# Performance work log

Hardware: AMD Instinct MI355X
Metric: run time of the kernel (lower is better)

The kernel has to match this reference:

```python
import jax, jax.numpy as jnp
import numpy as np

B = 16384
WIDE_DIM = 256          # 32 wide features * dim 8
DEEP_DIM = 1024         # 64 deep features * embedding_dim 16
SHARED = [2048, 1024, 512]
DOMAIN = [512, 256]
NUM_DOMAINS = 8


def setup_inputs() -> dict:
    key = jax.random.key(0)
    ks = jax.random.split(key, 20)
    s = 0.01  # embedding_init_var-style small init
    inp = {
        "wide_features": jax.random.normal(ks[0], (B, WIDE_DIM), jnp.float32),
        "deep_features": jax.random.normal(ks[1], (B, DEEP_DIM), jnp.float32),
        "domain_ids": jax.random.randint(ks[2], (B,), 0, NUM_DOMAINS, jnp.int64),
        # shared MLP (weights stored [in, out])
        "W1": jax.random.normal(ks[3], (DEEP_DIM, SHARED[0]), jnp.float32) * s,
        "b1": jnp.zeros((SHARED[0],), jnp.float32),
        "W2": jax.random.normal(ks[4], (SHARED[0], SHARED[1]), jnp.float32) * s,
        "b2": jnp.zeros((SHARED[1],), jnp.float32),
        "W3": jax.random.normal(ks[5], (SHARED[1], SHARED[2]), jnp.float32) * s,
        "b3": jnp.zeros((SHARED[2],), jnp.float32),
        # domain-specific MLP
        "Wd1": jax.random.normal(ks[6], (SHARED[2], DOMAIN[0]), jnp.float32) * s,
        "bd1": jnp.zeros((DOMAIN[0],), jnp.float32),
        "Wd2": jax.random.normal(ks[7], (DOMAIN[0], DOMAIN[1]), jnp.float32) * s,
        "bd2": jnp.zeros((DOMAIN[1],), jnp.float32),
        # per-domain output heads: Linear(DOMAIN[-1], 1) per domain
        "Wh": jax.random.normal(ks[8], (NUM_DOMAINS, DOMAIN[1]), jnp.float32) * s,
        "bh": jnp.zeros((NUM_DOMAINS,), jnp.float32),
    }
    return inp


def reference(wide_features, deep_features, domain_ids,
              W1, b1, W2, b2, W3, b3, Wd1, bd1, Wd2, bd2, Wh, bh):
    # wide part: sum embedding output to a scalar logit per sample [B, 1]
    wide = jnp.sum(wide_features, axis=1, keepdims=True)
    # shared deep MLP
    h = jax.nn.relu(deep_features @ W1 + b1)
    h = jax.nn.relu(h @ W2 + b2)
    shared = jax.nn.relu(h @ W3 + b3)          # [B, 512]
    # domain-specific tower (shared across domains)
    d = jax.nn.relu(shared @ Wd1 + bd1)
    d = jax.nn.relu(d @ Wd2 + bd2)             # [B, 256]
    # per-sample domain head routing: gather head weights, fused dot
    w = Wh[domain_ids]                          # [B, 256]
    head = jnp.sum(d * w, axis=1, keepdims=True) + bh[domain_ids][:, None]  # [B, 1]
    out = jax.nn.sigmoid(wide + head)
    return (out, shared, d)
```

## Files before the change

kernel.cpp:

```cpp
#include <hip/hip_runtime.h>
#include <hip/hip_bf16.h>


typedef __attribute__((ext_vector_type(8))) short short8;
typedef __attribute__((ext_vector_type(4))) float f32x4;

static __device__ __forceinline__ unsigned short f2bf_bits(float x) {
  __hip_bfloat16 h = __float2bfloat16(x);
  return __builtin_bit_cast(unsigned short, h);
}
static __device__ __forceinline__ float bf_bits2f(unsigned short u) {
  __hip_bfloat16 h = __builtin_bit_cast(__hip_bfloat16, u);
  return __bfloat162float(h);
}

static __device__ __forceinline__ void gload16(const void* g, void* l) {
  __builtin_amdgcn_global_load_lds(
      (const __attribute__((address_space(1))) void*)g,
      (__attribute__((address_space(3))) void*)l, 16, 0, 0);
}

static __device__ __forceinline__ unsigned lds_u32(const void* p) {
  return (unsigned)(uintptr_t)(const __attribute__((address_space(3))) void*)p;
}

static __device__ __forceinline__ short8 dsr(unsigned addr) {
  short8 r;
  asm volatile("ds_read_b128 %0, %1" : "=v"(r) : "v"(addr));
  return r;
}

#define MFMA16(a, b, c) __builtin_amdgcn_mfma_f32_16x16x32_bf16((a), (b), (c), 0, 0, 0)
#define SB0() __builtin_amdgcn_sched_barrier(0)
#define PRIO(x) __builtin_amdgcn_s_setprio(x)
#define BAR() __builtin_amdgcn_s_barrier()
#define MEMFENCE() asm volatile("" ::: "memory")

__global__ void transpose_convert(const float* __restrict__ W,
                                  __hip_bfloat16* __restrict__ Wt,
                                  int K, int N) {
  __shared__ float tile[64][65];
  const int k0 = blockIdx.y * 64;
  const int n0 = blockIdx.x * 64;
  const int t  = threadIdx.x;
  const int tn = t & 63;
  const int t4 = t >> 6;
#pragma unroll
  for (int p = 0; p < 16; ++p) {
    int kl = p * 4 + t4;
    tile[kl][tn] = W[(size_t)(k0 + kl) * N + (n0 + tn)];
  }
  __syncthreads();
#pragma unroll
  for (int p = 0; p < 16; ++p) {
    int nl = p * 4 + t4;
    Wt[(size_t)(n0 + nl) * K + (k0 + tn)] = __float2bfloat16(tile[tn][nl]);
  }
}

__global__ void f32_to_bf16(const float* __restrict__ in,
                            unsigned short* __restrict__ out, int n8) {
  int i = blockIdx.x * blockDim.x + threadIdx.x;
  if (i >= n8) return;
  const f32x4* p = (const f32x4*)in + (size_t)i * 2;
  f32x4 a = p[0], b = p[1];
  short8 o;
  o[0] = (short)f2bf_bits(a[0]); o[1] = (short)f2bf_bits(a[1]);
  o[2] = (short)f2bf_bits(a[2]); o[3] = (short)f2bf_bits(a[3]);
  o[4] = (short)f2bf_bits(b[0]); o[5] = (short)f2bf_bits(b[1]);
  o[6] = (short)f2bf_bits(b[2]); o[7] = (short)f2bf_bits(b[3]);
  *(short8*)(out + (size_t)i * 8) = o;
}

__global__ __launch_bounds__(512, 2) void gemm_2c(
    const __hip_bfloat16* __restrict__ A,
    const __hip_bfloat16* __restrict__ Bt,
    const float* __restrict__ bias,
    __hip_bfloat16* __restrict__ Cb,
    float* __restrict__ Cf,
    int N, int K, int nbx) {
  __shared__ char lds[131072];

  const int tid  = threadIdx.x;
  const int lane = tid & 63;
  const int wid  = tid >> 6;
  const int wm   = wid >> 2;
  const int wn   = wid & 3;

  const int nwg = gridDim.x;
  const int cpx = nwg >> 3;
  const int id  = blockIdx.x;
  const int swz = (id & 7) * cpx + (id >> 3);
  const int bm  = (swz / nbx) * 256;
  const int bn  = (swz % nbx) * 256;

  const int ln15 = lane & 15;
  const unsigned cswz = (unsigned)((((lane >> 4) ^ (lane & 7)) << 4));

  const unsigned aoff = (unsigned)((wm * 128 + ln15) * 128) + cswz;
  const unsigned boff = 32768u + (unsigned)((wn * 64 + ln15) * 128) + cswz;

  const int nt = K >> 6;

  const __hip_bfloat16* baseA = A  + (size_t)(bm + (tid >> 3)) * K +
                                ((tid & 7) ^ ((tid >> 3) & 7)) * 8;
  const __hip_bfloat16* baseB = Bt + (size_t)(bn + (tid >> 3)) * K +
                                ((tid & 7) ^ ((tid >> 3) & 7)) * 8;
  const unsigned ldst0 = (unsigned)(wid * 1024);

  auto stage = [&](int kt, int half, int isB) {
    const __hip_bfloat16* base = isB ? baseB : baseA;
    char* dst = lds + ((kt & 1) * 65536) + (isB ? 32768 : 0) + half * 16384;
#pragma unroll
    for (int q = 0; q < 2; ++q) {
      gload16(base + (size_t)((half * 128 + q * 64) * K + kt * 64),
              dst + q * 8192 + ldst0);
    }
  };

  auto LD = [&](unsigned off) -> short8 {
    return *(const short8*)&lds[off];
  };

  f32x4 acc[8][4] = {};
  short8 aLo[4][2], aHi[4][2], b0v[2][2], b1v[2][2];

  stage(0, 0, 1); stage(0, 0, 0); stage(0, 1, 1); stage(0, 1, 0);
  if (nt > 1) {
    stage(1, 0, 1); stage(1, 0, 0);
    asm volatile("s_waitcnt vmcnt(4)");
  } else {
    asm volatile("s_waitcnt vmcnt(0)");
  }
  BAR();
  MEMFENCE();
#pragma unroll
  for (int mi = 0; mi < 4; ++mi)
#pragma unroll
    for (int kk = 0; kk < 2; ++kk)
      aLo[mi][kk] = LD((aoff + (unsigned)(mi * 2048)) ^ (unsigned)(kk << 6));
#pragma unroll
  for (int nj = 0; nj < 2; ++nj)
#pragma unroll
    for (int kk = 0; kk < 2; ++kk)
      b0v[nj][kk] = LD((boff + (unsigned)(nj * 2048)) ^ (unsigned)(kk << 6));

  for (int t = 0; t < nt; ++t) {
    const unsigned po = (unsigned)(t & 1) * 65536u;
    const unsigned pn = po ^ 65536u;

#pragma unroll
    for (int nj = 0; nj < 2; ++nj)
#pragma unroll
      for (int kk = 0; kk < 2; ++kk)
        b1v[nj][kk] = LD((po + boff + (unsigned)((nj + 2) * 2048)) ^ (unsigned)(kk << 6));
    if (t + 1 < nt) stage(t + 1, 1, 1);
    PRIO(1);
#pragma unroll
    for (int kk = 0; kk < 2; ++kk)
#pragma unroll
      for (int mi = 0; mi < 4; ++mi)
#pragma unroll
        for (int nj = 0; nj < 2; ++nj)
          acc[mi][nj] = MFMA16(aLo[mi][kk], b0v[nj][kk], acc[mi][nj]);
    PRIO(0);

#pragma unroll
    for (int mi = 0; mi < 4; ++mi)
#pragma unroll
      for (int kk = 0; kk < 2; ++kk)
        aHi[mi][kk] = LD((po + aoff + (unsigned)((mi + 4) * 2048)) ^ (unsigned)(kk << 6));
    if (t + 1 < nt) stage(t + 1, 1, 0);
    PRIO(1);
#pragma unroll
    for (int kk = 0; kk < 2; ++kk)
#pragma unroll
      for (int mi = 0; mi < 4; ++mi)
#pragma unroll
        for (int nj = 0; nj < 2; ++nj)
          acc[mi][nj + 2] = MFMA16(aLo[mi][kk], b1v[nj][kk], acc[mi][nj + 2]);
    PRIO(0);
    BAR();
    MEMFENCE();

    PRIO(1);
#pragma unroll
    for (int kk = 0; kk < 2; ++kk)
#pragma unroll
      for (int mi = 0; mi < 4; ++mi)
#pragma unroll
        for (int nj = 0; nj < 2; ++nj)
          acc[mi + 4][nj] = MFMA16(aHi[mi][kk], b0v[nj][kk], acc[mi + 4][nj]);
    PRIO(0);
    if (t + 2 < nt) stage(t + 2, 0, 1);
    if (t + 1 < nt) {
      if (t + 2 < nt) asm volatile("s_waitcnt vmcnt(2)");
      else            asm volatile("s_waitcnt vmcnt(0)");
      BAR();
      MEMFENCE();
    }

    if (t + 1 < nt) {
#pragma unroll
      for (int mi = 0; mi < 4; ++mi)
#pragma unroll
        for (int kk = 0; kk < 2; ++kk)
          aLo[mi][kk] = LD((pn + aoff + (unsigned)(mi * 2048)) ^ (unsigned)(kk << 6));
#pragma unroll
      for (int nj = 0; nj < 2; ++nj)
#pragma unroll
        for (int kk = 0; kk < 2; ++kk)
          b0v[nj][kk] = LD((pn + boff + (unsigned)(nj * 2048)) ^ (unsigned)(kk << 6));
    }
    PRIO(1);
#pragma unroll
    for (int kk = 0; kk < 2; ++kk)
#pragma unroll
      for (int mi = 0; mi < 4; ++mi)
#pragma unroll
        for (int nj = 0; nj < 2; ++nj)
          acc[mi + 4][nj + 2] = MFMA16(aHi[mi][kk], b1v[nj][kk], acc[mi + 4][nj + 2]);
    PRIO(0);
    if (t + 2 < nt) stage(t + 2, 0, 0);
  }

  float biasv[4];
#pragma unroll
  for (int nj = 0; nj < 4; ++nj)
    biasv[nj] = bias[bn + wn * 64 + nj * 16 + ln15];

#pragma unroll
  for (int mi = 0; mi < 8; ++mi) {
    int row0 = bm + wm * 128 + mi * 16 + (lane >> 4) * 4;
#pragma unroll
    for (int nj = 0; nj < 4; ++nj) {
      int col = bn + wn * 64 + nj * 16 + ln15;
#pragma unroll
      for (int r = 0; r < 4; ++r) {
        float v = acc[mi][nj][r] + biasv[nj];
        v = v > 0.f ? v : 0.f;
        size_t idx = (size_t)(row0 + r) * N + col;
        Cb[idx] = __float2bfloat16(v);
        if (Cf) Cf[idx] = v;
      }
    }
  }
}

__global__ __launch_bounds__(512, 2) void gemm_128(
    const __hip_bfloat16* __restrict__ A,
    const __hip_bfloat16* __restrict__ Bt,
    const float* __restrict__ bias,
    __hip_bfloat16* __restrict__ Cb,
    float* __restrict__ Cf,
    int N, int K, int nbx) {
  __shared__ char lds[98304];

  const int tid  = threadIdx.x;
  const int lane = tid & 63;
  const int wid  = tid >> 6;
  const int wm   = wid >> 2;
  const int wn   = wid & 3;

  const int nwg = gridDim.x;
  const int cpx = nwg >> 3;
  const int id  = blockIdx.x;
  const int swz = (id & 7) * cpx + (id >> 3);
  const int bm  = (swz / nbx) * 128;
  const int bn  = (swz % nbx) * 256;

  const int ln15 = lane & 15;
  const unsigned cswz = (unsigned)((((lane >> 4) ^ (lane & 7)) << 4));

  const unsigned lbase = lds_u32(lds);
  const unsigned arow0 = lbase + (unsigned)(wm * 64 + ln15) * 128u + cswz;
  const unsigned brow0 = lbase + 16384u + (unsigned)(wn * 64 + ln15) * 128u + cswz;

  const int nt = K >> 6;

  const int swc = (tid & 7) ^ ((tid >> 3) & 7);
  const __hip_bfloat16* baseA = A  + (size_t)(bm + (tid >> 3)) * K + swc * 8;
  const __hip_bfloat16* baseB = Bt + (size_t)(bn + (tid >> 3)) * K + swc * 8;
  const unsigned ldst0 = (unsigned)(tid * 16);

  auto stageA = [&](int kt, int half) {
    char* dst = lds + ((kt & 1) * 49152) + half * 8192;
    gload16(baseA + (size_t)((half * 64) * K + kt * 64), dst + ldst0);
  };
  auto stageB = [&](int kt, int half) {
    char* dst = lds + ((kt & 1) * 49152) + 16384 + half * 16384;
#pragma unroll
    for (int q = 0; q < 2; ++q) {
      gload16(baseB + (size_t)((half * 128 + q * 64) * K + kt * 64),
              dst + q * 8192 + ldst0);
    }
  };

  f32x4 acc[4][4] = {};
  short8 aLo[2][2], aHi[2][2], b0v[2][2], b1v[2][2];

  stageB(0, 0); stageA(0, 0); stageB(0, 1); stageA(0, 1);
  if (nt > 1) {
    stageB(1, 0); stageA(1, 0);
    asm volatile("s_waitcnt vmcnt(3)");
  } else {
    asm volatile("s_waitcnt vmcnt(0)");
  }
  BAR();
#pragma unroll
  for (int mi = 0; mi < 2; ++mi) {
    unsigned ad = arow0 + (unsigned)(mi * 2048);
    aLo[mi][0] = dsr(ad); aLo[mi][1] = dsr(ad ^ 64u);
  }

  for (int t = 0; t < nt; ++t) {
    const unsigned po = (unsigned)(t & 1) * 49152u;
    const unsigned pn = po ^ 49152u;

    asm volatile("s_waitcnt lgkmcnt(0)");
    SB0();
#pragma unroll
    for (int nj = 0; nj < 2; ++nj) b0v[nj][0] = dsr(brow0 + po + (unsigned)(nj * 2048));
#pragma unroll
    for (int nj = 0; nj < 2; ++nj) b0v[nj][1] = dsr((brow0 + po + (unsigned)(nj * 2048)) ^ 64u);
#pragma unroll
    for (int nj = 0; nj < 2; ++nj) b1v[nj][0] = dsr(brow0 + po + (unsigned)((nj + 2) * 2048));
#pragma unroll
    for (int nj = 0; nj < 2; ++nj) b1v[nj][1] = dsr((brow0 + po + (unsigned)((nj + 2) * 2048)) ^ 64u);
    if (t + 1 < nt) stageB(t + 1, 1);
    asm volatile("s_waitcnt lgkmcnt(6)");
    SB0();
    PRIO(1);
#pragma unroll
    for (int mi = 0; mi < 2; ++mi)
#pragma unroll
      for (int nj = 0; nj < 2; ++nj)
        acc[mi][nj] = MFMA16(aLo[mi][0], b0v[nj][0], acc[mi][nj]);
    asm volatile("s_waitcnt lgkmcnt(4)");
    SB0();
#pragma unroll
    for (int mi = 0; mi < 2; ++mi)
#pragma unroll
      for (int nj = 0; nj < 2; ++nj)
        acc[mi][nj] = MFMA16(aLo[mi][1], b0v[nj][1], acc[mi][nj]);
    PRIO(0);

#pragma unroll
    for (int mi = 0; mi < 2; ++mi) {
      unsigned ad = arow0 + po + (unsigned)((mi + 2) * 2048);
      aHi[mi][0] = dsr(ad); aHi[mi][1] = dsr(ad ^ 64u);
    }
    if (t + 1 < nt) stageA(t + 1, 1);
    asm volatile("s_waitcnt lgkmcnt(4)");
    SB0();
    PRIO(1);
#pragma unroll
    for (int kk = 0; kk < 2; ++kk)
#pragma unroll
      for (int mi = 0; mi < 2; ++mi)
#pragma unroll
        for (int nj = 0; nj < 2; ++nj)
          acc[mi][nj + 2] = MFMA16(aLo[mi][kk], b1v[nj][kk], acc[mi][nj + 2]);
    PRIO(0);
    BAR();

    asm volatile("s_waitcnt lgkmcnt(0)");
    SB0();
    PRIO(1);
#pragma unroll
    for (int kk = 0; kk < 2; ++kk)
#pragma unroll
      for (int mi = 0; mi < 2; ++mi)
#pragma unroll
        for (int nj = 0; nj < 2; ++nj)
          acc[mi + 2][nj] = MFMA16(aHi[mi][kk], b0v[nj][kk], acc[mi + 2][nj]);
    PRIO(0);
    if (t + 2 < nt) stageB(t + 2, 0);
    if (t + 2 < nt)      asm volatile("s_waitcnt vmcnt(2)");
    else if (t + 1 < nt) asm volatile("s_waitcnt vmcnt(0)");
    if (t + 1 < nt) BAR();

    if (t + 1 < nt) {
#pragma unroll
      for (int mi = 0; mi < 2; ++mi) {
        unsigned ad = arow0 + pn + (unsigned)(mi * 2048);
        aLo[mi][0] = dsr(ad); aLo[mi][1] = dsr(ad ^ 64u);
      }
    }
    SB0();
    PRIO(1);
#pragma unroll
    for (int kk = 0; kk < 2; ++kk)
#pragma unroll
      for (int mi = 0; mi < 2; ++mi)
#pragma unroll
        for (int nj = 0; nj < 2; ++nj)
          acc[mi + 2][nj + 2] = MFMA16(aHi[mi][kk], b1v[nj][kk], acc[mi + 2][nj + 2]);
    PRIO(0);
    if (t + 2 < nt) stageA(t + 2, 0);
  }

  float biasv[4];
#pragma unroll
  for (int nj = 0; nj < 4; ++nj)
    biasv[nj] = bias[bn + wn * 64 + nj * 16 + ln15];

#pragma unroll
  for (int mi = 0; mi < 4; ++mi) {
    int row0 = bm + wm * 64 + mi * 16 + (lane >> 4) * 4;
#pragma unroll
    for (int nj = 0; nj < 4; ++nj) {
      int col = bn + wn * 64 + nj * 16 + ln15;
#pragma unroll
      for (int r = 0; r < 4; ++r) {
        float v = acc[mi][nj][r] + biasv[nj];
        v = v > 0.f ? v : 0.f;
        size_t idx = (size_t)(row0 + r) * N + col;
        Cb[idx] = __float2bfloat16(v);
        if (Cf) Cf[idx] = v;
      }
    }
  }
}

__global__ __launch_bounds__(256, 2) void gemm_bt(
    const __hip_bfloat16* __restrict__ A,
    const __hip_bfloat16* __restrict__ Bt,
    const float* __restrict__ bias,
    __hip_bfloat16* __restrict__ Cb,
    float* __restrict__ Cf,
    int N, int K) {
  __shared__ char lds[32768];

  const int tid  = threadIdx.x;
  const int lane = tid & 63;
  const int wid  = tid >> 6;
  const int wm   = wid >> 1;
  const int wn   = wid & 1;
  const int bm   = blockIdx.y * 128;
  const int bn   = blockIdx.x * 128;

  f32x4 acc[4][4] = {};

  const int srow = tid >> 3;
  const int sk   = (tid & 7) * 8;
  const int kTiles = K >> 6;

  for (int kt = 0; kt < kTiles; ++kt) {
    __syncthreads();
    const __hip_bfloat16* ga = A  + (size_t)(bm + srow) * K + kt * 64 + sk;
    const __hip_bfloat16* gb = Bt + (size_t)(bn + srow) * K + kt * 64 + sk;
#pragma unroll
    for (int p = 0; p < 4; ++p) {
      gload16(ga + (size_t)(p * 32) * K, &lds[p * 4096 + wid * 1024]);
      gload16(gb + (size_t)(p * 32) * K, &lds[16384 + p * 4096 + wid * 1024]);
    }
    __syncthreads();

#pragma unroll
    for (int kk = 0; kk < 2; ++kk) {
      short8 avec[4], bvec[4];
#pragma unroll
      for (int i = 0; i < 4; ++i) {
        int row = wm * 64 + i * 16 + (lane & 15);
        avec[i] = *(const short8*)&lds[row * 128 + kk * 64 + (lane >> 4) * 16];
      }
#pragma unroll
      for (int j = 0; j < 4; ++j) {
        int row = wn * 64 + j * 16 + (lane & 15);
        bvec[j] = *(const short8*)&lds[16384 + row * 128 + kk * 64 + (lane >> 4) * 16];
      }
#pragma unroll
      for (int i = 0; i < 4; ++i)
#pragma unroll
        for (int j = 0; j < 4; ++j)
          acc[i][j] = MFMA16(avec[i], bvec[j], acc[i][j]);
    }
  }

  float biasv[4];
#pragma unroll
  for (int j = 0; j < 4; ++j)
    biasv[j] = bias[bn + wn * 64 + j * 16 + (lane & 15)];

#pragma unroll
  for (int i = 0; i < 4; ++i) {
    int row0 = bm + wm * 64 + i * 16 + (lane >> 4) * 4;
#pragma unroll
    for (int j = 0; j < 4; ++j) {
      int col = bn + wn * 64 + j * 16 + (lane & 15);
#pragma unroll
      for (int r = 0; r < 4; ++r) {
        float v = acc[i][j][r] + biasv[j];
        v = v > 0.f ? v : 0.f;
        size_t idx = (size_t)(row0 + r) * N + col;
        Cb[idx] = __float2bfloat16(v);
        if (Cf) Cf[idx] = v;
      }
    }
  }
}

__global__ __launch_bounds__(256) void head_kernel(
    const float* __restrict__ wide,
    const __hip_bfloat16* __restrict__ D,
    const int* __restrict__ dom,
    const float* __restrict__ Wh,
    const float* __restrict__ bh,
    float* __restrict__ out, int B) {
  const int wid  = threadIdx.x >> 6;
  const int lane = threadIdx.x & 63;
  const int row  = blockIdx.x * 4 + wid;
  if (row >= B) return;
  const int dm = dom[row];

  f32x4 wv = ((const f32x4*)(wide + (size_t)row * 256))[lane];
  float tot = wv[0] + wv[1] + wv[2] + wv[3];

  const unsigned short* drow = (const unsigned short*)(D + (size_t)row * 256);
  ushort4 dv = ((const ushort4*)drow)[lane];
  f32x4 hv = ((const f32x4*)(Wh + (size_t)dm * 256))[lane];
  tot += bf_bits2f(dv.x) * hv[0] + bf_bits2f(dv.y) * hv[1] +
         bf_bits2f(dv.z) * hv[2] + bf_bits2f(dv.w) * hv[3];

#pragma unroll
  for (int off = 32; off > 0; off >>= 1) tot += __shfl_xor(tot, off);

  if (lane == 0) {
    float x = tot + bh[dm];
    out[row] = 1.f / (1.f + __expf(-x));
  }
}

extern "C" void kernel_launch(void* const* d_in, const int* in_sizes, int n_in,
                              void* d_out, int out_size, void* d_ws, size_t ws_size,
                              hipStream_t stream) {
  const float* wide = (const float*)d_in[0];
  const float* deep = (const float*)d_in[1];
  const int*   dom  = (const int*)d_in[2];
  const float* W1  = (const float*)d_in[3];
  const float* b1  = (const float*)d_in[4];
  const float* W2  = (const float*)d_in[5];
  const float* b2  = (const float*)d_in[6];
  const float* W3  = (const float*)d_in[7];
  const float* b3  = (const float*)d_in[8];
  const float* Wd1 = (const float*)d_in[9];
  const float* bd1 = (const float*)d_in[10];
  const float* Wd2 = (const float*)d_in[11];
  const float* bd2 = (const float*)d_in[12];
  const float* Wh  = (const float*)d_in[13];
  const float* bh  = (const float*)d_in[14];
  float* out = (float*)d_out;

  const int B = 16384;
  char* ws = (char*)d_ws;
  __hip_bfloat16* buf0 = (__hip_bfloat16*)ws;
  __hip_bfloat16* buf1 = (__hip_bfloat16*)(ws + 33554432ull);
  __hip_bfloat16* W1t  = (__hip_bfloat16*)(ws + 100663296ull);
  __hip_bfloat16* W2t  = W1t + 2048 * 1024;
  __hip_bfloat16* W3t  = W2t + 1024 * 2048;
  __hip_bfloat16* Wd1t = W3t + 512 * 1024;
  __hip_bfloat16* Wd2t = Wd1t + 512 * 512;

  transpose_convert<<<dim3(2048 / 64, 1024 / 64), 256, 0, stream>>>(W1, W1t, 1024, 2048);
  transpose_convert<<<dim3(1024 / 64, 2048 / 64), 256, 0, stream>>>(W2, W2t, 2048, 1024);
  transpose_convert<<<dim3(512 / 64, 1024 / 64), 256, 0, stream>>>(W3, W3t, 1024, 512);
  transpose_convert<<<dim3(512 / 64, 512 / 64), 256, 0, stream>>>(Wd1, Wd1t, 512, 512);
  transpose_convert<<<dim3(256 / 64, 512 / 64), 256, 0, stream>>>(Wd2, Wd2t, 512, 256);

  {
    int n8 = B * 1024 / 8;
    f32_to_bf16<<<(n8 + 255) / 256, 256, 0, stream>>>(deep, (unsigned short*)buf0, n8);
  }

  float* shared_out = out + B;
  float* d_out_f    = out + B + (size_t)B * 512;

  gemm_2c<<<dim3((2048 / 256) * (B / 256)), 512, 0, stream>>>(
      buf0, W1t, b1, buf1, nullptr, 2048, 1024, 2048 / 256);
  gemm_2c<<<dim3((1024 / 256) * (B / 256)), 512, 0, stream>>>(
      buf1, W2t, b2, buf0, nullptr, 1024, 2048, 1024 / 256);
  gemm_128<<<dim3((B / 128) * (512 / 256)), 512, 0, stream>>>(
      buf0, W3t, b3, buf1, shared_out, 512, 1024, 512 / 256);
  gemm_128<<<dim3((B / 128) * (512 / 256)), 512, 0, stream>>>(
      buf1, Wd1t, bd1, buf0, nullptr, 512, 512, 512 / 256);
  gemm_bt<<<dim3(256 / 128, B / 128), 256, 0, stream>>>(buf0, Wd2t, bd2, buf1, d_out_f, 256, 512);

  head_kernel<<<B / 4, 256, 0, stream>>>(wide, buf1, dom, Wh, bh, out, B);
}
```

Before: 224.3 us.

## Fuse last tower GEMM with domain head and deepen prefetch staging

The final 512->256 GEMM and the separate head kernel are replaced by one pipelined GEMM kernel. Each block covers a 128-row by full-256-column tile, keeps the bf16 activations in LDS, and computes the wide sum, domain head dot product and sigmoid in its epilogue. This removes a kernel launch and the bf16 write and re-read of the d activations. Separately, the two existing GEMM kernels now prefetch both halves of a K tile together two steps ahead, with adjusted vmcnt waits, which raises the number of global loads in flight per thread.

Measured after the change: 218.9 us. -2.4%, faster.

```diff
diff --git a/kernel.cpp b/kernel.cpp
--- a/kernel.cpp
+++ b/kernel.cpp
@@ -125,10 +125,10 @@
   f32x4 acc[8][4] = {};
   short8 aLo[4][2], aHi[4][2], b0v[2][2], b1v[2][2];
 
-  stage(0, 0, 1); stage(0, 0, 0); stage(0, 1, 1); stage(0, 1, 0);
+  stage(0, 0, 1); stage(0, 1, 1); stage(0, 0, 0); stage(0, 1, 0);
   if (nt > 1) {
-    stage(1, 0, 1); stage(1, 0, 0);
-    asm volatile("s_waitcnt vmcnt(4)");
+    stage(1, 0, 1); stage(1, 1, 1); stage(1, 0, 0); stage(1, 1, 0);
+    asm volatile("s_waitcnt vmcnt(8)");
   } else {
     asm volatile("s_waitcnt vmcnt(0)");
   }
@@ -154,7 +154,6 @@
 #pragma unroll
       for (int kk = 0; kk < 2; ++kk)
         b1v[nj][kk] = LD((po + boff + (unsigned)((nj + 2) * 2048)) ^ (unsigned)(kk << 6));
-    if (t + 1 < nt) stage(t + 1, 1, 1);
     PRIO(1);
 #pragma unroll
     for (int kk = 0; kk < 2; ++kk)
@@ -170,7 +169,6 @@
 #pragma unroll
       for (int kk = 0; kk < 2; ++kk)
         aHi[mi][kk] = LD((po + aoff + (unsigned)((mi + 4) * 2048)) ^ (unsigned)(kk << 6));
-    if (t + 1 < nt) stage(t + 1, 1, 0);
     PRIO(1);
 #pragma unroll
     for (int kk = 0; kk < 2; ++kk)
@@ -192,9 +190,9 @@
         for (int nj = 0; nj < 2; ++nj)
           acc[mi + 4][nj] = MFMA16(aHi[mi][kk], b0v[nj][kk], acc[mi + 4][nj]);
     PRIO(0);
-    if (t + 2 < nt) stage(t + 2, 0, 1);
+    if (t + 2 < nt) { stage(t + 2, 0, 1); stage(t + 2, 1, 1); }
     if (t + 1 < nt) {
-      if (t + 2 < nt) asm volatile("s_waitcnt vmcnt(2)");
+      if (t + 2 < nt) asm volatile("s_waitcnt vmcnt(4)");
       else            asm volatile("s_waitcnt vmcnt(0)");
       BAR();
       MEMFENCE();
@@ -221,7 +219,7 @@
         for (int nj = 0; nj < 2; ++nj)
           acc[mi + 4][nj + 2] = MFMA16(aHi[mi][kk], b1v[nj][kk], acc[mi + 4][nj + 2]);
     PRIO(0);
-    if (t + 2 < nt) stage(t + 2, 0, 0);
+    if (t + 2 < nt) { stage(t + 2, 0, 0); stage(t + 2, 1, 0); }
   }
 
   float biasv[4];
@@ -299,10 +297,10 @@
   f32x4 acc[4][4] = {};
   short8 aLo[2][2], aHi[2][2], b0v[2][2], b1v[2][2];
 
-  stageB(0, 0); stageA(0, 0); stageB(0, 1); stageA(0, 1);
+  stageB(0, 0); stageB(0, 1); stageA(0, 0); stageA(0, 1);
   if (nt > 1) {
-    stageB(1, 0); stageA(1, 0);
-    asm volatile("s_waitcnt vmcnt(3)");
+    stageB(1, 0); stageB(1, 1); stageA(1, 0); stageA(1, 1);
+    asm volatile("s_waitcnt vmcnt(6)");
   } else {
     asm volatile("s_waitcnt vmcnt(0)");
   }
@@ -327,7 +325,6 @@
     for (int nj = 0; nj < 2; ++nj) b1v[nj][0] = dsr(brow0 + po + (unsigned)((nj + 2) * 2048));
 #pragma unroll
     for (int nj = 0; nj < 2; ++nj) b1v[nj][1] = dsr((brow0 + po + (unsigned)((nj + 2) * 2048)) ^ 64u);
-    if (t + 1 < nt) stageB(t + 1, 1);
     asm volatile("s_waitcnt lgkmcnt(6)");
     SB0();
     PRIO(1);
@@ -350,7 +347,6 @@
       unsigned ad = arow0 + po + (unsigned)((mi + 2) * 2048);
       aHi[mi][0] = dsr(ad); aHi[mi][1] = dsr(ad ^ 64u);
     }
-    if (t + 1 < nt) stageA(t + 1, 1);
     asm volatile("s_waitcnt lgkmcnt(4)");
     SB0();
     PRIO(1);
@@ -375,10 +371,12 @@
         for (int nj = 0; nj < 2; ++nj)
           acc[mi + 2][nj] = MFMA16(aHi[mi][kk], b0v[nj][kk], acc[mi + 2][nj]);
     PRIO(0);
-    if (t + 2 < nt) stageB(t + 2, 0);
-    if (t + 2 < nt)      asm volatile("s_waitcnt vmcnt(2)");
-    else if (t + 1 < nt) asm volatile("s_waitcnt vmcnt(0)");
-    if (t + 1 < nt) BAR();
+    if (t + 2 < nt) { stageB(t + 2, 0); stageB(t + 2, 1); }
+    if (t + 1 < nt) {
+      if (t + 2 < nt) asm volatile("s_waitcnt vmcnt(4)");
+      else            asm volatile("s_waitcnt vmcnt(0)");
+      BAR();
+    }
 
     if (t + 1 < nt) {
 #pragma unroll
@@ -397,7 +395,7 @@
         for (int nj = 0; nj < 2; ++nj)
           acc[mi + 2][nj + 2] = MFMA16(aHi[mi][kk], b1v[nj][kk], acc[mi + 2][nj + 2]);
     PRIO(0);
-    if (t + 2 < nt) stageA(t + 2, 0);
+    if (t + 2 < nt) { stageA(t + 2, 0); stageA(t + 2, 1); }
   }
 
   float biasv[4];
@@ -423,112 +421,231 @@
   }
 }
 
-__global__ __launch_bounds__(256, 2) void gemm_bt(
+__global__ __launch_bounds__(512, 2) void gemm_l5h(
     const __hip_bfloat16* __restrict__ A,
     const __hip_bfloat16* __restrict__ Bt,
     const float* __restrict__ bias,
-    __hip_bfloat16* __restrict__ Cb,
-    float* __restrict__ Cf,
-    int N, int K) {
-  __shared__ char lds[32768];
+    float* __restrict__ Df,
+    const float* __restrict__ wide,
+    const int* __restrict__ dom,
+    const float* __restrict__ Wh,
+    const float* __restrict__ bh,
+    float* __restrict__ outp,
+    int K) {
+  __shared__ char lds[98304];
 
   const int tid  = threadIdx.x;
   const int lane = tid & 63;
   const int wid  = tid >> 6;
-  const int wm   = wid >> 1;
-  const int wn   = wid & 1;
-  const int bm   = blockIdx.y * 128;
-  const int bn   = blockIdx.x * 128;
+  const int wm   = wid >> 2;
+  const int wn   = wid & 3;
+
+  const int nwg = gridDim.x;
+  const int cpx = nwg >> 3;
+  const int id  = blockIdx.x;
+  const int swz = (id & 7) * cpx + (id >> 3);
+  const int bm  = swz * 128;
+
+  const int ln15 = lane & 15;
+  const unsigned cswz = (unsigned)((((lane >> 4) ^ (lane & 7)) << 4));
+
+  const unsigned lbase = lds_u32(lds);
+  const unsigned arow0 = lbase + (unsigned)(wm * 64 + ln15) * 128u + cswz;
+  const unsigned brow0 = lbase + 16384u + (unsigned)(wn * 64 + ln15) * 128u + cswz;
+
+  const int nt = K >> 6;
+
+  const int swc = (tid & 7) ^ ((tid >> 3) & 7);
+  const __hip_bfloat16* baseA = A  + (size_t)(bm + (tid >> 3)) * K + swc * 8;
+  const __hip_bfloat16* baseB = Bt + (size_t)(tid >> 3) * K + swc * 8;
+  const unsigned ldst0 = (unsigned)(tid * 16);
+
+  auto stageA = [&](int kt, int half) {
+    char* dst = lds + ((kt & 1) * 49152) + half * 8192;
+    gload16(baseA + (size_t)((half * 64) * K + kt * 64), dst + ldst0);
+  };
+  auto stageB = [&](int kt, int half) {
+    char* dst = lds + ((kt & 1) * 49152) + 16384 + half * 16384;
+#pragma unroll
+    for (int q = 0; q < 2; ++q) {
+      gload16(baseB + (size_t)((half * 128 + q * 64) * K + kt * 64),
+              dst + q * 8192 + ldst0);
+    }
+  };
 
   f32x4 acc[4][4] = {};
-
-  const int srow = tid >> 3;
-  const int sk   = (tid & 7) * 8;
-  const int kTiles = K >> 6;
-
-  for (int kt = 0; kt < kTiles; ++kt) {
-    __syncthreads();
-    const __hip_bfloat16* ga = A  + (size_t)(bm + srow) * K + kt * 64 + sk;
-    const __hip_bfloat16* gb = Bt + (size_t)(bn + srow) * K + kt * 64 + sk;
-#pragma unroll
-    for (int p = 0; p < 4; ++p) {
-      gload16(ga + (size_t)(p * 32) * K, &lds[p * 4096 + wid * 1024]);
-      gload16(gb + (size_t)(p * 32) * K, &lds[16384 + p * 4096 + wid * 1024]);
-    }
-    __syncthreads();
-
-#pragma unroll
-    for (int kk = 0; kk < 2; ++kk) {
-      short8 avec[4], bvec[4];
-#pragma unroll
-      for (int i = 0; i < 4; ++i) {
-        int row = wm * 64 + i * 16 + (lane & 15);
-        avec[i] = *(const short8*)&lds[row * 128 + kk * 64 + (lane >> 4) * 16];
+  short8 aLo[2][2], aHi[2][2], b0v[2][2], b1v[2][2];
+
+  stageB(0, 0); stageB(0, 1); stageA(0, 0); stageA(0, 1);
+  if (nt > 1) {
+    stageB(1, 0); stageB(1, 1); stageA(1, 0); stageA(1, 1);
+    asm volatile("s_waitcnt vmcnt(6)");
+  } else {
+    asm volatile("s_waitcnt vmcnt(0)");
+  }
+  BAR();
+#pragma unroll
+  for (int mi = 0; mi < 2; ++mi) {
+    unsigned ad = arow0 + (unsigned)(mi * 2048);
+    aLo[mi][0] = dsr(ad); aLo[mi][1] = dsr(ad ^ 64u);
+  }
+
+  for (int t = 0; t < nt; ++t) {
+    const unsigned po = (unsigned)(t & 1) * 49152u;
+    const unsigned pn = po ^ 49152u;
+
+    asm volatile("s_waitcnt lgkmcnt(0)");
+    SB0();
+#pragma unroll
+    for (int nj = 0; nj < 2; ++nj) b0v[nj][0] = dsr(brow0 + po + (unsigned)(nj * 2048));
+#pragma unroll
+    for (int nj = 0; nj < 2; ++nj) b0v[nj][1] = dsr((brow0 + po + (unsigned)(nj * 2048)) ^ 64u);
+#pragma unroll
+    for (int nj = 0; nj < 2; ++nj) b1v[nj][0] = dsr(brow0 + po + (unsigned)((nj + 2) * 2048));
+#pragma unroll
+    for (int nj = 0; nj < 2; ++nj) b1v[nj][1] = dsr((brow0 + po + (unsigned)((nj + 2) * 2048)) ^ 64u);
+    asm volatile("s_waitcnt lgkmcnt(6)");
+    SB0();
+    PRIO(1);
+#pragma unroll
+    for (int mi = 0; mi < 2; ++mi)
+#pragma unroll
+      for (int nj = 0; nj < 2; ++nj)
+        acc[mi][nj] = MFMA16(aLo[mi][0], b0v[nj][0], acc[mi][nj]);
+    asm volatile("s_waitcnt lgkmcnt(4)");
+    SB0();
+#pragma unroll
+    for (int mi = 0; mi < 2; ++mi)
+#pragma unroll
+      for (int nj = 0; nj < 2; ++nj)
+        acc[mi][nj] = MFMA16(aLo[mi][1], b0v[nj][1], acc[mi][nj]);
+    PRIO(0);
+
+#pragma unroll
+    for (int mi = 0; mi < 2; ++mi) {
+      unsigned ad = arow0 + po + (unsigned)((mi + 2) * 2048);
+      aHi[mi][0] = dsr(ad); aHi[mi][1] = dsr(ad ^ 64u);
+    }
+    asm volatile("s_waitcnt lgkmcnt(4)");
+    SB0();
+    PRIO(1);
+#pragma unroll
+    for (int kk = 0; kk < 2; ++kk)
+#pragma unroll
+      for (int mi = 0; mi < 2; ++mi)
+#pragma unroll
+        for (int nj = 0; nj < 2; ++nj)
+          acc[mi][nj + 2] = MFMA16(aLo[mi][kk], b1v[nj][kk], acc[mi][nj + 2]);
+    PRIO(0);
+    BAR();
+
+    asm volatile("s_waitcnt lgkmcnt(0)");
+    SB0();
+    PRIO(1);
+#pragma unroll
+    for (int kk = 0; kk < 2; ++kk)
+#pragma unroll
+      for (int mi = 0; mi < 2; ++mi)
+#pragma unroll
+        for (int nj = 0; nj < 2; ++nj)
+          acc[mi + 2][nj] = MFMA16(aHi[mi][kk], b0v[nj][kk], acc[mi + 2][nj]);
+    PRIO(0);
+    if (t + 2 < nt) { stageB(t + 2, 0); stageB(t + 2, 1); }
+    if (t + 1 < nt) {
+      if (t + 2 < nt) asm volatile("s_waitcnt vmcnt(4)");
+      else            asm volatile("s_waitcnt vmcnt(0)");
+      BAR();
+    }
+
+    if (t + 1 < nt) {
+#pragma unroll
+      for (int mi = 0; mi < 2; ++mi) {
+        unsigned ad = arow0 + pn + (unsigned)(mi * 2048);
+        aLo[mi][0] = dsr(ad); aLo[mi][1] = dsr(ad ^ 64u);
       }
-#pragma unroll
-      for (int j = 0; j < 4; ++j) {
-        int row = wn * 64 + j * 16 + (lane & 15);
-        bvec[j] = *(const short8*)&lds[16384 + row * 128 + kk * 64 + (lane >> 4) * 16];
+    }
+    SB0();
+    PRIO(1);
+#pragma unroll
+    for (int kk = 0; kk < 2; ++kk)
+#pragma unroll
+      for (int mi = 0; mi < 2; ++mi)
+#pragma unroll
+        for (int nj = 0; nj < 2; ++nj)
+          acc[mi + 2][nj + 2] = MFMA16(aHi[mi][kk], b1v[nj][kk], acc[mi + 2][nj + 2]);
+    PRIO(0);
+    if (t + 2 < nt) { stageA(t + 2, 0); stageA(t + 2, 1); }
+  }
+
+  BAR();
+  MEMFENCE();
+  unsigned short* ldsD = (unsigned short*)lds;
+  float* ldsH = (float*)(lds + 128 * 264 * 2);
+
+  float biasv[4];
+#pragma unroll
+  for (int nj = 0; nj < 4; ++nj)
+    biasv[nj] = bias[wn * 64 + nj * 16 + ln15];
+
+#pragma unroll
+  for (int mi = 0; mi < 4; ++mi) {
+    int lrow0 = wm * 64 + mi * 16 + (lane >> 4) * 4;
+#pragma unroll
+    for (int nj = 0; nj < 4; ++nj) {
+      int col = wn * 64 + nj * 16 + ln15;
+#pragma unroll
+      for (int r = 0; r < 4; ++r) {
+        float v = acc[mi][nj][r] + biasv[nj];
+        v = v > 0.f ? v : 0.f;
+        Df[(size_t)(bm + lrow0 + r) * 256 + col] = v;
+        ldsD[(lrow0 + r) * 264 + col] = f2bf_bits(v);
       }
-#pragma unroll
-      for (int i = 0; i < 4; ++i)
-#pragma unroll
-        for (int j = 0; j < 4; ++j)
-          acc[i][j] = MFMA16(avec[i], bvec[j], acc[i][j]);
-    }
-  }
-
-  float biasv[4];
-#pragma unroll
-  for (int j = 0; j < 4; ++j)
-    biasv[j] = bias[bn + wn * 64 + j * 16 + (lane & 15)];
-
-#pragma unroll
-  for (int i = 0; i < 4; ++i) {
-    int row0 = bm + wm * 64 + i * 16 + (lane >> 4) * 4;
-#pragma unroll
-    for (int j = 0; j < 4; ++j) {
-      int col = bn + wn * 64 + j * 16 + (lane & 15);
-#pragma unroll
-      for (int r = 0; r < 4; ++r) {
-        float v = acc[i][j][r] + biasv[j];
-        v = v > 0.f ? v : 0.f;
-        size_t idx = (size_t)(row0 + r) * N + col;
-        Cb[idx] = __float2bfloat16(v);
-        if (Cf) Cf[idx] = v;
-      }
-    }
-  }
-}
-
-__global__ __launch_bounds__(256) void head_kernel(
-    const float* __restrict__ wide,
-    const __hip_bfloat16* __restrict__ D,
-    const int* __restrict__ dom,
-    const float* __restrict__ Wh,
-    const float* __restrict__ bh,
-    float* __restrict__ out, int B) {
-  const int wid  = threadIdx.x >> 6;
-  const int lane = threadIdx.x & 63;
-  const int row  = blockIdx.x * 4 + wid;
-  if (row >= B) return;
-  const int dm = dom[row];
-
-  f32x4 wv = ((const f32x4*)(wide + (size_t)row * 256))[lane];
-  float tot = wv[0] + wv[1] + wv[2] + wv[3];
-
-  const unsigned short* drow = (const unsigned short*)(D + (size_t)row * 256);
-  ushort4 dv = ((const ushort4*)drow)[lane];
-  f32x4 hv = ((const f32x4*)(Wh + (size_t)dm * 256))[lane];
-  tot += bf_bits2f(dv.x) * hv[0] + bf_bits2f(dv.y) * hv[1] +
-         bf_bits2f(dv.z) * hv[2] + bf_bits2f(dv.w) * hv[3];
-
-#pragma unroll
-  for (int off = 32; off > 0; off >>= 1) tot += __shfl_xor(tot, off);
-
-  if (lane == 0) {
-    float x = tot + bh[dm];
-    out[row] = 1.f / (1.f + __expf(-x));
+    }
+  }
+
+  const int erow = tid >> 2;
+  const int eq   = tid & 3;
+  float s = 0.f;
+  {
+    const f32x4* wp = (const f32x4*)(wide + (size_t)(bm + erow) * 256 + eq * 64);
+#pragma unroll
+    for (int j = 0; j < 16; ++j) {
+      f32x4 w = wp[j];
+      s += w[0] + w[1] + w[2] + w[3];
+    }
+  }
+  BAR();
+  MEMFENCE();
+
+  const int dm = dom[bm + erow];
+  float h = 0.f;
+  {
+    const f32x4* hp = (const f32x4*)(Wh + (size_t)dm * 256 + eq * 64);
+    const short8* dp = (const short8*)(ldsD + erow * 264 + eq * 64);
+#pragma unroll
+    for (int j = 0; j < 8; ++j) {
+      short8 d8 = dp[j];
+      f32x4 h0 = hp[j * 2], h1 = hp[j * 2 + 1];
+      h += bf_bits2f((unsigned short)d8[0]) * h0[0] +
+           bf_bits2f((unsigned short)d8[1]) * h0[1] +
+           bf_bits2f((unsigned short)d8[2]) * h0[2] +
+           bf_bits2f((unsigned short)d8[3]) * h0[3] +
+           bf_bits2f((unsigned short)d8[4]) * h1[0] +
+           bf_bits2f((unsigned short)d8[5]) * h1[1] +
+           bf_bits2f((unsigned short)d8[6]) * h1[2] +
+           bf_bits2f((unsigned short)d8[7]) * h1[3];
+    }
+  }
+  ldsH[erow * 4 + eq] = s + h;
+  BAR();
+  MEMFENCE();
+
+  if (tid < 128) {
+    float val = ldsH[tid * 4] + ldsH[tid * 4 + 1] +
+                ldsH[tid * 4 + 2] + ldsH[tid * 4 + 3];
+    int dmr = dom[bm + tid];
+    float x = val + bh[dmr];
+    outp[bm + tid] = 1.f / (1.f + __expf(-x));
   }
 }
 
@@ -584,7 +701,6 @@
       buf0, W3t, b3, buf1, shared_out, 512, 1024, 512 / 256);
   gemm_128<<<dim3((B / 128) * (512 / 256)), 512, 0, stream>>>(
       buf1, Wd1t, bd1, buf0, nullptr, 512, 512, 512 / 256);
-  gemm_bt<<<dim3(256 / 128, B / 128), 256, 0, stream>>>(buf0, Wd2t, bd2, buf1, d_out_f, 256, 512);
-
-  head_kernel<<<B / 4, 256, 0, stream>>>(wide, buf1, dom, Wh, bh, out, B);
-}
+  gemm_l5h<<<dim3(B / 128), 512, 0, stream>>>(
+      buf0, Wd2t, bd2, d_out_f, wide, dom, Wh, bh, out, 512);
+}
```
